# Performance work log

Measured on AMD Instinct MI355X. Metric: run time of the kernel, lower is better.

## Reference

```python
import jax, jax.numpy as jnp
from jax import lax
import numpy as np

O = 64      # out_channels (== in_channels == groups, depthwise)
P = 3       # prompt_len
K = 17      # prompt_size (large kernel size)
RANK = 4
# (small_kernel_size, pixel_unshuffle_scale, dilations) for prompt_size=17
CONFIGS = [(3, 4, (4, 5, 7)), (5, 2, (1,)), (9, 1, (2,))]


def conv2d(x, w, b=None, stride=1, padding=0, dilation=1, groups=1):
    out = lax.conv_general_dilated(
        x, w, (stride, stride), [(padding, padding)] * 2,
        rhs_dilation=(dilation, dilation), feature_group_count=groups,
        dimension_numbers=('NCHW', 'OIHW', 'NCHW'))
    return out if b is None else out + b[None, :, None, None]


def pixel_unshuffle(x, s):
    n, c, h, w = x.shape
    x = x.reshape(n, c, h // s, s, w // s, s)
    return x.transpose(0, 1, 3, 5, 2, 4).reshape(n, c * s * s, h // s, w // s)


def bilinear(x, oh, ow):
    # F.interpolate(mode='bilinear', align_corners=False); all uses downsample
    n, c, h, w = x.shape
    def coords(o, i):
        src = jnp.clip((jnp.arange(o, dtype=jnp.float32) + 0.5) * (i / o) - 0.5, 0.0, i - 1.0)
        i0 = jnp.floor(src).astype(jnp.int32)
        i1 = jnp.minimum(i0 + 1, i - 1)
        return i0, i1, src - i0.astype(jnp.float32)
    y0, y1, ty = coords(oh, h)
    x0, x1, tx = coords(ow, w)
    r0, r1 = x[:, :, y0], x[:, :, y1]
    top = r0[:, :, :, x0] * (1 - tx) + r0[:, :, :, x1] * tx
    bot = r1[:, :, :, x0] * (1 - tx) + r1[:, :, :, x1] * tx
    ty = ty[:, None]
    return top * (1 - ty) + bot * ty


def zero_interleave(k, d):
    # conv_transpose2d with 1x1 ones kernel, stride d == insert d-1 zeros
    o, c, ks, _ = k.shape
    e = d * (ks - 1) + 1
    return jnp.zeros((o, c, e, e), k.dtype).at[:, :, ::d, ::d].set(k)


def _branch(weight0, k_size, scale, dils, dw_w, dw_b, w1, b1, w2, b2, dilw, merged):
    w = weight0
    if scale > 1:
        ph = (-K) % scale
        w = jnp.pad(w, ((0, 0), (0, 0), (0, ph), (0, ph)))
        w = pixel_unshuffle(w, scale)
    h = conv2d(w, dw_w, dw_b, padding=1, groups=dw_w.shape[0])  # depthwise 3x3
    h = jax.nn.relu(conv2d(h, w1, b1))                          # 1x1 expand
    h = conv2d(h, w2, b2)                                       # 1x1 project
    h = bilinear(h, k_size, k_size)                             # (O, P*scale_or_P, k, k)
    for idx, d in enumerate(dils):
        dk = jnp.einsum('ochw,pc->ophw', h, dilw[idx])          # 1x1, no bias -> (O,P,k,k)
        eq = zero_interleave(dk, d)
        p = K // 2 - eq.shape[-1] // 2
        merged = merged + jnp.pad(eq, ((0, 0), (0, 0), (p, p), (p, p)))
    return merged


def _forward(x, A1, A2, A3, B1, B2, B3,
             dw_w3, dw_b3, w1_3, b1_3, w2_3, b2_3, dilw3,
             dw_w5, dw_b5, w1_5, b1_5, w2_5, b2_5, dilw5,
             dw_w9, dw_b9, w1_9, b1_9, w2_9, b2_9, dilw9):
    # low-rank reconstruction: (O,1,K,r) @ (O,1,r,K) -> (O,1,K,K), cat -> (O,P,K,K)
    weight0 = jnp.concatenate(
        [jnp.einsum('oikj,oijl->oikl', A, B) for A, B in ((A1, B1), (A2, B2), (A3, B3))],
        axis=1)
    merged = jnp.zeros_like(weight0)
    packs = [(dw_w3, dw_b3, w1_3, b1_3, w2_3, b2_3, dilw3),
             (dw_w5, dw_b5, w1_5, b1_5, w2_5, b2_5, dilw5),
             (dw_w9, dw_b9, w1_9, b1_9, w2_9, b2_9, dilw9)]
    for (k_size, scale, dils), pk in zip(CONFIGS, packs):
        merged = _branch(weight0, k_size, scale, dils, *pk, merged)
    w = merged.reshape(O * P, 1, K, K)
    return conv2d(x, w, padding=K // 2, groups=64)  # depthwise, 3 filters per channel


def setup_inputs() -> dict:
    key = jax.random.key(0)
    ks = iter(jax.random.split(key, 64))
    def rn(shape, s=0.05):
        return jax.random.normal(next(ks), shape, jnp.float32) * s
    inp = {'x': jax.random.normal(next(ks), (8, 64, 256, 256), jnp.float32)}
    for i in (1, 2, 3):
        inp[f'A{i}'] = rn((O, 1, K, RANK), 0.2)
        inp[f'B{i}'] = rn((O, 1, RANK, K), 0.2)
    # (pixel_unshuffle channels, hidden, mlp_out, n_dilations) per kernel size
    specs = {3: (48, 64, 12, 3), 5: (12, 48, 6, 1), 9: (3, 12, 3, 1)}
    for kk, (c, hid, out_c, nd) in specs.items():
        inp[f'dw_w{kk}'] = rn((c, 1, 3, 3))
        inp[f'dw_b{kk}'] = rn((c,))
        inp[f'w1_{kk}'] = rn((hid, c, 1, 1))
        inp[f'b1_{kk}'] = rn((hid,))
        inp[f'w2_{kk}'] = rn((out_c, hid, 1, 1))
        inp[f'b2_{kk}'] = rn((out_c,))
        inp[f'dilw{kk}'] = rn((nd, P, out_c))
    return inp


def reference(x, A1, A2, A3, B1, B2, B3,
              dw_w3, dw_b3, w1_3, b1_3, w2_3, b2_3, dilw3,
              dw_w5, dw_b5, w1_5, b1_5, w2_5, b2_5, dilw5,
              dw_w9, dw_b9, w1_9, b1_9, w2_9, b2_9, dilw9):
    return _forward(x, A1, A2, A3, B1, B2, B3,
                    dw_w3, dw_b3, w1_3, b1_3, w2_3, b2_3, dilw3,
                    dw_w5, dw_b5, w1_5, b1_5, w2_5, b2_5, dilw5,
                    dw_w9, dw_b9, w1_9, b1_9, w2_9, b2_9, dilw9)
```

## Files before the change

kernel.cpp:

```cpp
#include <hip/hip_runtime.h>
#include <cstddef>

typedef _Float16 h8 __attribute__((ext_vector_type(8)));
typedef float f4 __attribute__((ext_vector_type(4)));
typedef unsigned int uint32;

struct BranchP {
  int ksz, scale, CIN, HID, COUT, S, nd;
  int dils[3];
  const float *dw_w, *dw_b, *w1, *b1, *w2, *b2, *dilw;
};

__device__ void run_branch(int tid, const BranchP P,
                           const float* w0, float* merged,
                           float* bufA, float* bufB) {
  const int S = P.S, ksz = P.ksz, CIN = P.CIN, HID = P.HID, COUT = P.COUT;
  const int SS = S * S;
  for (int i = tid; i < CIN * SS; i += 256) {
    const int cc = i / SS, rem = i % SS, hh = rem / S, ww = rem % S;
    const int s2 = P.scale * P.scale;
    const int c = cc / s2, r2 = cc % s2, si = r2 / P.scale, sj = r2 % P.scale;
    const int sh = hh * P.scale + si, sw = ww * P.scale + sj;
    bufA[i] = (sh < 17 && sw < 17) ? w0[c * 289 + sh * 17 + sw] : 0.f;
  }
  __syncthreads();
  for (int i = tid; i < CIN * SS; i += 256) {
    const int ch = i / SS, rem = i % SS, y = rem / S, x = rem % S;
    float acc = P.dw_b[ch];
    for (int u = 0; u < 3; ++u)
      for (int v = 0; v < 3; ++v) {
        const int yy = y + u - 1, xx = x + v - 1;
        if (yy >= 0 && yy < S && xx >= 0 && xx < S)
          acc += bufA[ch * SS + yy * S + xx] * P.dw_w[ch * 9 + u * 3 + v];
      }
    bufB[i] = acc;
  }
  __syncthreads();
  for (int i = tid; i < HID * SS; i += 256) {
    const int ho = i / SS, rem = i % SS;
    float acc = P.b1[ho];
    for (int ci = 0; ci < CIN; ++ci) acc += bufB[ci * SS + rem] * P.w1[ho * CIN + ci];
    bufA[i] = fmaxf(acc, 0.f);
  }
  __syncthreads();
  for (int i = tid; i < COUT * SS; i += 256) {
    const int po = i / SS, rem = i % SS;
    float acc = P.b2[po];
    for (int ci = 0; ci < HID; ++ci) acc += bufA[ci * SS + rem] * P.w2[po * HID + ci];
    bufB[i] = acc;
  }
  __syncthreads();
  for (int i = tid; i < COUT * ksz * ksz; i += 256) {
    const int c = i / (ksz * ksz), rem = i % (ksz * ksz), oy = rem / ksz, ox = rem % ksz;
    const float ratio = (float)S / (float)ksz;
    float sy = fminf(fmaxf((oy + 0.5f) * ratio - 0.5f, 0.f), (float)(S - 1));
    float sx = fminf(fmaxf((ox + 0.5f) * ratio - 0.5f, 0.f), (float)(S - 1));
    const int y0 = (int)sy; const int y1 = min(y0 + 1, S - 1); const float ty = sy - (float)y0;
    const int x0 = (int)sx; const int x1 = min(x0 + 1, S - 1); const float tx = sx - (float)x0;
    const float* img = bufB + c * SS;
    const float top = img[y0 * S + x0] * (1.f - tx) + img[y0 * S + x1] * tx;
    const float bot = img[y1 * S + x0] * (1.f - tx) + img[y1 * S + x1] * tx;
    bufA[i] = top * (1.f - ty) + bot * ty;
  }
  __syncthreads();
  for (int di = 0; di < P.nd; ++di) {
    const int d = P.dils[di];
    const int e = d * (ksz - 1) + 1, pp = 8 - e / 2;
    for (int i = tid; i < 3 * ksz * ksz; i += 256) {
      const int p = i / (ksz * ksz), rem = i % (ksz * ksz), ih = rem / ksz, iw = rem % ksz;
      float acc = 0.f;
      for (int c2 = 0; c2 < COUT; ++c2)
        acc += bufA[c2 * ksz * ksz + rem] * P.dilw[(di * 3 + p) * COUT + c2];
      merged[p * 289 + (pp + d * ih) * 17 + (pp + d * iw)] += acc;
    }
  }
  __syncthreads();
}

#define KPAD 416
#define ACH (2 * 16 * KPAD)

__global__ __launch_bounds__(256) void prep_kernel(
    const float* __restrict__ A1, const float* __restrict__ B1,
    const float* __restrict__ A2, const float* __restrict__ B2,
    const float* __restrict__ A3, const float* __restrict__ B3,
    const float* __restrict__ dw_w3, const float* __restrict__ dw_b3,
    const float* __restrict__ w1_3, const float* __restrict__ b1_3,
    const float* __restrict__ w2_3, const float* __restrict__ b2_3,
    const float* __restrict__ dilw3,
    const float* __restrict__ dw_w5, const float* __restrict__ dw_b5,
    const float* __restrict__ w1_5, const float* __restrict__ b1_5,
    const float* __restrict__ w2_5, const float* __restrict__ b2_5,
    const float* __restrict__ dilw5,
    const float* __restrict__ dw_w9, const float* __restrict__ dw_b9,
    const float* __restrict__ w1_9, const float* __restrict__ b1_9,
    const float* __restrict__ w2_9, const float* __restrict__ b2_9,
    const float* __restrict__ dilw9,
    _Float16* __restrict__ wA) {
  const int o = blockIdx.x;
  const int tid = threadIdx.x;
  __shared__ float w0[3 * 289];
  __shared__ float merged[3 * 289];
  __shared__ float bufA[3888];
  __shared__ float bufB[3888];

  for (int i = tid; i < 3 * 289; i += 256) {
    const int c = i / 289, rem = i % 289, k = rem / 17, l = rem % 17;
    const float* A = (c == 0 ? A1 : (c == 1 ? A2 : A3)) + o * 68;
    const float* B = (c == 0 ? B1 : (c == 1 ? B2 : B3)) + o * 68;
    float s = 0.f;
    for (int r = 0; r < 4; ++r) s += A[k * 4 + r] * B[r * 17 + l];
    w0[i] = s;
    merged[i] = 0.f;
  }
  __syncthreads();

  {
    BranchP P{3, 4, 48, 64, 12, 5, 3, {4, 5, 7}, dw_w3, dw_b3, w1_3, b1_3, w2_3, b2_3, dilw3};
    run_branch(tid, P, w0, merged, bufA, bufB);
  }
  {
    BranchP P{5, 2, 12, 48, 6, 9, 1, {1, 0, 0}, dw_w5, dw_b5, w1_5, b1_5, w2_5, b2_5, dilw5};
    run_branch(tid, P, w0, merged, bufA, bufB);
  }
  {
    BranchP P{9, 1, 3, 12, 3, 17, 1, {2, 0, 0}, dw_w9, dw_b9, w1_9, b1_9, w2_9, b2_9, dilw9};
    run_branch(tid, P, w0, merged, bufA, bufB);
  }

  for (int i = tid; i < ACH; i += 256) {
    const int g = i / (16 * KPAD);
    const int m = (i / KPAD) % 16;
    const int k = i % KPAD;
    const int dxi = k / 24, r = k % 24;
    int pp, yo;
    if (g == 0) { pp = m & 1; yo = m >> 1; } else { pp = 2; yo = m; }
    const int dy = r - 8 - yo;
    float val = 0.f;
    if (!(g == 1 && m >= 8) && dy >= -8 && dy <= 8 && dxi <= 16)
      val = merged[pp * 289 + (dy + 8) * 17 + dxi];
    wA[(size_t)o * ACH + i] = (_Float16)val;
  }
}

__global__ __launch_bounds__(256) void conv_mfma_kernel(
    const float* __restrict__ xin, const _Float16* __restrict__ wA,
    float* __restrict__ out) {
  const int wid = ((blockIdx.x & 7) << 9) + (blockIdx.x >> 3);
  const int n   = wid >> 9;
  const int ch  = (wid >> 3) & 63;
  const int yg  = (wid & 7) * 32;
  const int tid = threadIdx.x;

#define PITCH 56
  __shared__ __align__(16) _Float16 Xt[280 * PITCH];

  const float* xim = xin + ((size_t)(n * 64 + ch)) * 65536;

  const int lane = tid & 63;
  const int wv = tid >> 6;
  const int row = lane & 15;
  const int kg = lane >> 4;

  h8 a1[13], a2[13];
  {
    const _Float16* Ab = wA + (size_t)ch * ACH + row * KPAD;
    #pragma unroll
    for (int t = 0; t < 13; ++t) {
      const int k0 = t * 32 + kg * 8;
      a1[t] = __builtin_bit_cast(h8, *(const uint4*)(Ab + k0));
      a2[t] = __builtin_bit_cast(h8, *(const uint4*)(Ab + 16 * KPAD + k0));
    }
  }

  for (int i = tid; i < 4 * 280; i += 256) {
    const int rb = i / 280, c = i % 280;
    const int gx = c - 8;
    const bool cok = (gx >= 0 && gx < 256);
    float v[8];
    #pragma unroll
    for (int rr = 0; rr < 8; ++rr) {
      const int gy = yg - 8 + rb * 8 + rr;
      v[rr] = (cok && gy >= 0 && gy < 256) ? xim[gy * 256 + gx] : 0.f;
    }
    uint4 u;
    u.x = __builtin_bit_cast(uint32, __builtin_amdgcn_cvt_pkrtz(v[0], v[1]));
    u.y = __builtin_bit_cast(uint32, __builtin_amdgcn_cvt_pkrtz(v[2], v[3]));
    u.z = __builtin_bit_cast(uint32, __builtin_amdgcn_cvt_pkrtz(v[4], v[5]));
    u.w = __builtin_bit_cast(uint32, __builtin_amdgcn_cvt_pkrtz(v[6], v[7]));
    *(uint4*)&Xt[c * PITCH + rb * 8] = u;
  }
  __syncthreads();

  float pbv[3][8];
  int pbc[3], pbrb[3];
  #pragma unroll
  for (int q = 0; q < 3; ++q) {
    const int i = tid + q * 256;
    pbc[q] = -1;
    if (i < 2 * 280) {
      const int rb = 4 + i / 280, c = i % 280;
      pbc[q] = c; pbrb[q] = rb;
      const int gx = c - 8;
      const bool cok = (gx >= 0 && gx < 256);
      #pragma unroll
      for (int rr = 0; rr < 8; ++rr) {
        const int gy = yg - 8 + rb * 8 + rr;
        pbv[q][rr] = (cok && gy >= 0 && gy < 256) ? xim[gy * 256 + gx] : 0.f;
      }
    }
  }

  int boff[13];
  #pragma unroll
  for (int t = 0; t < 13; ++t) {
    const int k0 = t * 32 + kg * 8;
    const int dxi = k0 / 24, r0 = k0 - dxi * 24;
    boff[t] = (row + dxi) * PITCH + r0;
  }

#define DO_PAIR(pr) do {                                                       \
    const int g_ = (pr) >> 1, cp_ = (pr) & 1;                                  \
    const int j0a_ = (wv * 4 + cp_ * 2) * 16;                                  \
    const int ba_ = j0a_ * PITCH + 8 * g_;                                     \
    const int bb_ = ba_ + 16 * PITCH;                                          \
    f4 c1a = {0.f,0.f,0.f,0.f}, c2a = {0.f,0.f,0.f,0.f};                       \
    f4 c1b = {0.f,0.f,0.f,0.f}, c2b = {0.f,0.f,0.f,0.f};                       \
    _Pragma("unroll")                                                          \
    for (int t = 0; t < 13; ++t) {                                             \
      const h8 vba = __builtin_bit_cast(h8, *(const uint4*)&Xt[ba_ + boff[t]]);\
      const h8 vbb = __builtin_bit_cast(h8, *(const uint4*)&Xt[bb_ + boff[t]]);\
      c1a = __builtin_amdgcn_mfma_f32_16x16x32_f16(a1[t], vba, c1a, 0, 0, 0);  \
      c1b = __builtin_amdgcn_mfma_f32_16x16x32_f16(a1[t], vbb, c1b, 0, 0, 0);  \
      c2a = __builtin_amdgcn_mfma_f32_16x16x32_f16(a2[t], vba, c2a, 0, 0, 0);  \
      c2b = __builtin_amdgcn_mfma_f32_16x16x32_f16(a2[t], vbb, c2b, 0, 0, 0);  \
    }                                                                          \
    const int ygg_ = yg + 8 * g_;                                              \
    _Pragma("unroll")                                                          \
    for (int half = 0; half < 2; ++half) {                                     \
      const int gx_ = j0a_ + half * 16 + row;                                  \
      const f4 s1 = half ? c1b : c1a;                                          \
      const f4 s2 = half ? c2b : c2a;                                          \
      _Pragma("unroll")                                                        \
      for (int reg = 0; reg < 4; ++reg) {                                      \
        const int r_ = kg * 4 + reg;                                           \
        out[(((size_t)n * 192 + ch * 3 + (r_ & 1)) * 256 + (ygg_ + (r_ >> 1))) * 256 + gx_] = s1[reg]; \
      }                                                                        \
      if (kg < 2) {                                                            \
        _Pragma("unroll")                                                      \
        for (int reg = 0; reg < 4; ++reg) {                                    \
          const int r_ = kg * 4 + reg;                                         \
          out[(((size_t)n * 192 + ch * 3 + 2) * 256 + (ygg_ + r_)) * 256 + gx_] = s2[reg]; \
        }                                                                      \
      }                                                                        \
    }                                                                          \
  } while (0)

  DO_PAIR(0); DO_PAIR(1);

  #pragma unroll
  for (int q = 0; q < 3; ++q) {
    if (pbc[q] >= 0) {
      uint4 u;
      u.x = __builtin_bit_cast(uint32, __builtin_amdgcn_cvt_pkrtz(pbv[q][0], pbv[q][1]));
      u.y = __builtin_bit_cast(uint32, __builtin_amdgcn_cvt_pkrtz(pbv[q][2], pbv[q][3]));
      u.z = __builtin_bit_cast(uint32, __builtin_amdgcn_cvt_pkrtz(pbv[q][4], pbv[q][5]));
      u.w = __builtin_bit_cast(uint32, __builtin_amdgcn_cvt_pkrtz(pbv[q][6], pbv[q][7]));
      *(uint4*)&Xt[pbc[q] * PITCH + pbrb[q] * 8] = u;
    }
  }

  DO_PAIR(2); DO_PAIR(3);

  __syncthreads();

  DO_PAIR(4); DO_PAIR(5); DO_PAIR(6); DO_PAIR(7);

#undef DO_PAIR
#undef PITCH
}

extern "C" void kernel_launch(void* const* d_in, const int* in_sizes, int n_in,
                              void* d_out, int out_size, void* d_ws, size_t ws_size,
                              hipStream_t stream) {
  const float* xin = (const float*)d_in[0];
  const float* A1 = (const float*)d_in[1];
  const float* B1 = (const float*)d_in[2];
  const float* A2 = (const float*)d_in[3];
  const float* B2 = (const float*)d_in[4];
  const float* A3 = (const float*)d_in[5];
  const float* B3 = (const float*)d_in[6];
  const float* dw_w3 = (const float*)d_in[7];
  const float* dw_b3 = (const float*)d_in[8];
  const float* w1_3 = (const float*)d_in[9];
  const float* b1_3 = (const float*)d_in[10];
  const float* w2_3 = (const float*)d_in[11];
  const float* b2_3 = (const float*)d_in[12];
  const float* dilw3 = (const float*)d_in[13];
  const float* dw_w5 = (const float*)d_in[14];
  const float* dw_b5 = (const float*)d_in[15];
  const float* w1_5 = (const float*)d_in[16];
  const float* b1_5 = (const float*)d_in[17];
  const float* w2_5 = (const float*)d_in[18];
  const float* b2_5 = (const float*)d_in[19];
  const float* dilw5 = (const float*)d_in[20];
  const float* dw_w9 = (const float*)d_in[21];
  const float* dw_b9 = (const float*)d_in[22];
  const float* w1_9 = (const float*)d_in[23];
  const float* b1_9 = (const float*)d_in[24];
  const float* w2_9 = (const float*)d_in[25];
  const float* b2_9 = (const float*)d_in[26];
  const float* dilw9 = (const float*)d_in[27];

  _Float16* wA = (_Float16*)d_ws;

  prep_kernel<<<64, 256, 0, stream>>>(
      A1, B1, A2, B2, A3, B3,
      dw_w3, dw_b3, w1_3, b1_3, w2_3, b2_3, dilw3,
      dw_w5, dw_b5, w1_5, b1_5, w2_5, b2_5, dilw5,
      dw_w9, dw_b9, w1_9, b1_9, w2_9, b2_9, dilw9,
      wA);

  conv_mfma_kernel<<<dim3(4096), 256, 0, stream>>>(xin, wA, (float*)d_out);
}
```

Before: 214.4 us.

## Cut register pressure: stream second weight tile from memory, drop split prefetch

The second A-operand weight tile is no longer kept in registers. It is reloaded from global memory in staged groups inside each pair computation, and the kernel now asks for 3 blocks per SM via launch bounds. The register prefetch of the lower input rows, with its mid-kernel LDS write and extra barrier, is replaced by loading all 6 row blocks before a single barrier. The aim is to free VGPRs for higher occupancy. The cost is repeated global/L2 weight loads per pair and the loss of overlap between the second input load and the MFMA work.

```diff
diff --git a/kernel.cpp b/kernel.cpp
--- a/kernel.cpp
+++ b/kernel.cpp
@@ -143,7 +143,7 @@
   }
 }
 
-__global__ __launch_bounds__(256) void conv_mfma_kernel(
+__global__ __launch_bounds__(256, 3) void conv_mfma_kernel(
     const float* __restrict__ xin, const _Float16* __restrict__ wA,
     float* __restrict__ out) {
   const int wid = ((blockIdx.x & 7) << 9) + (blockIdx.x >> 3);
@@ -162,18 +162,14 @@
   const int row = lane & 15;
   const int kg = lane >> 4;
 
-  h8 a1[13], a2[13];
-  {
-    const _Float16* Ab = wA + (size_t)ch * ACH + row * KPAD;
-    #pragma unroll
-    for (int t = 0; t < 13; ++t) {
-      const int k0 = t * 32 + kg * 8;
-      a1[t] = __builtin_bit_cast(h8, *(const uint4*)(Ab + k0));
-      a2[t] = __builtin_bit_cast(h8, *(const uint4*)(Ab + 16 * KPAD + k0));
-    }
-  }
-
-  for (int i = tid; i < 4 * 280; i += 256) {
+  const _Float16* Ab = wA + (size_t)ch * ACH + row * KPAD;
+  const _Float16* A2p = Ab + 16 * KPAD + kg * 8;
+  h8 a1[13];
+  #pragma unroll
+  for (int t = 0; t < 13; ++t)
+    a1[t] = __builtin_bit_cast(h8, *(const uint4*)(Ab + t * 32 + kg * 8));
+
+  for (int i = tid; i < 6 * 280; i += 256) {
     const int rb = i / 280, c = i % 280;
     const int gx = c - 8;
     const bool cok = (gx >= 0 && gx < 256);
@@ -192,25 +188,6 @@
   }
   __syncthreads();
 
-  float pbv[3][8];
-  int pbc[3], pbrb[3];
-  #pragma unroll
-  for (int q = 0; q < 3; ++q) {
-    const int i = tid + q * 256;
-    pbc[q] = -1;
-    if (i < 2 * 280) {
-      const int rb = 4 + i / 280, c = i % 280;
-      pbc[q] = c; pbrb[q] = rb;
-      const int gx = c - 8;
-      const bool cok = (gx >= 0 && gx < 256);
-      #pragma unroll
-      for (int rr = 0; rr < 8; ++rr) {
-        const int gy = yg - 8 + rb * 8 + rr;
-        pbv[q][rr] = (cok && gy >= 0 && gy < 256) ? xim[gy * 256 + gx] : 0.f;
-      }
-    }
-  }
-
   int boff[13];
   #pragma unroll
   for (int t = 0; t < 13; ++t) {
@@ -218,6 +195,17 @@
     const int dxi = k0 / 24, r0 = k0 - dxi * 24;
     boff[t] = (row + dxi) * PITCH + r0;
   }
+
+#define A2LD(t) __builtin_bit_cast(h8, *(const uint4*)(A2p + (t) * 32))
+
+#define MSTEP(t, a2v) do {                                                     \
+    const h8 vba = __builtin_bit_cast(h8, *(const uint4*)&Xt[ba_ + boff[t]]);  \
+    const h8 vbb = __builtin_bit_cast(h8, *(const uint4*)&Xt[bb_ + boff[t]]);  \
+    c1a = __builtin_amdgcn_mfma_f32_16x16x32_f16(a1[t], vba, c1a, 0, 0, 0);    \
+    c1b = __builtin_amdgcn_mfma_f32_16x16x32_f16(a1[t], vbb, c1b, 0, 0, 0);    \
+    c2a = __builtin_amdgcn_mfma_f32_16x16x32_f16((a2v), vba, c2a, 0, 0, 0);    \
+    c2b = __builtin_amdgcn_mfma_f32_16x16x32_f16((a2v), vbb, c2b, 0, 0, 0);    \
+  } while (0)
 
 #define DO_PAIR(pr) do {                                                       \
     const int g_ = (pr) >> 1, cp_ = (pr) & 1;                                  \
@@ -226,57 +214,41 @@
     const int bb_ = ba_ + 16 * PITCH;                                          \
     f4 c1a = {0.f,0.f,0.f,0.f}, c2a = {0.f,0.f,0.f,0.f};                       \
     f4 c1b = {0.f,0.f,0.f,0.f}, c2b = {0.f,0.f,0.f,0.f};                       \
-    _Pragma("unroll")                                                          \
-    for (int t = 0; t < 13; ++t) {                                             \
-      const h8 vba = __builtin_bit_cast(h8, *(const uint4*)&Xt[ba_ + boff[t]]);\
-      const h8 vbb = __builtin_bit_cast(h8, *(const uint4*)&Xt[bb_ + boff[t]]);\
-      c1a = __builtin_amdgcn_mfma_f32_16x16x32_f16(a1[t], vba, c1a, 0, 0, 0);  \
-      c1b = __builtin_amdgcn_mfma_f32_16x16x32_f16(a1[t], vbb, c1b, 0, 0, 0);  \
-      c2a = __builtin_amdgcn_mfma_f32_16x16x32_f16(a2[t], vba, c2a, 0, 0, 0);  \
-      c2b = __builtin_amdgcn_mfma_f32_16x16x32_f16(a2[t], vbb, c2b, 0, 0, 0);  \
-    }                                                                          \
+    h8 s0 = A2LD(0), s1 = A2LD(1), s2 = A2LD(2), s3 = A2LD(3);                 \
+    h8 s4 = A2LD(4), s5 = A2LD(5), s6 = A2LD(6);                               \
+    MSTEP(0, s0); MSTEP(1, s1); MSTEP(2, s2); MSTEP(3, s3);                    \
+    s0 = A2LD(7); s1 = A2LD(8); s2 = A2LD(9);                                  \
+    s3 = A2LD(10); h8 s7 = A2LD(11), s8 = A2LD(12);                            \
+    MSTEP(4, s4); MSTEP(5, s5); MSTEP(6, s6);                                  \
+    MSTEP(7, s0); MSTEP(8, s1); MSTEP(9, s2);                                  \
+    MSTEP(10, s3); MSTEP(11, s7); MSTEP(12, s8);                               \
     const int ygg_ = yg + 8 * g_;                                              \
     _Pragma("unroll")                                                          \
     for (int half = 0; half < 2; ++half) {                                     \
       const int gx_ = j0a_ + half * 16 + row;                                  \
-      const f4 s1 = half ? c1b : c1a;                                          \
-      const f4 s2 = half ? c2b : c2a;                                          \
+      const f4 t1 = half ? c1b : c1a;                                          \
+      const f4 t2 = half ? c2b : c2a;                                          \
       _Pragma("unroll")                                                        \
       for (int reg = 0; reg < 4; ++reg) {                                      \
         const int r_ = kg * 4 + reg;                                           \
-        out[(((size_t)n * 192 + ch * 3 + (r_ & 1)) * 256 + (ygg_ + (r_ >> 1))) * 256 + gx_] = s1[reg]; \
+        out[(((size_t)n * 192 + ch * 3 + (r_ & 1)) * 256 + (ygg_ + (r_ >> 1))) * 256 + gx_] = t1[reg]; \
       }                                                                        \
       if (kg < 2) {                                                            \
         _Pragma("unroll")                                                      \
         for (int reg = 0; reg < 4; ++reg) {                                    \
           const int r_ = kg * 4 + reg;                                         \
-          out[(((size_t)n * 192 + ch * 3 + 2) * 256 + (ygg_ + r_)) * 256 + gx_] = s2[reg]; \
+          out[(((size_t)n * 192 + ch * 3 + 2) * 256 + (ygg_ + r_)) * 256 + gx_] = t2[reg]; \
         }                                                                      \
       }                                                                        \
     }                                                                          \
   } while (0)
 
-  DO_PAIR(0); DO_PAIR(1);
-
-  #pragma unroll
-  for (int q = 0; q < 3; ++q) {
-    if (pbc[q] >= 0) {
-      uint4 u;
-      u.x = __builtin_bit_cast(uint32, __builtin_amdgcn_cvt_pkrtz(pbv[q][0], pbv[q][1]));
-      u.y = __builtin_bit_cast(uint32, __builtin_amdgcn_cvt_pkrtz(pbv[q][2], pbv[q][3]));
-      u.z = __builtin_bit_cast(uint32, __builtin_amdgcn_cvt_pkrtz(pbv[q][4], pbv[q][5]));
-      u.w = __builtin_bit_cast(uint32, __builtin_amdgcn_cvt_pkrtz(pbv[q][6], pbv[q][7]));
-      *(uint4*)&Xt[pbc[q] * PITCH + pbrb[q] * 8] = u;
-    }
-  }
-
-  DO_PAIR(2); DO_PAIR(3);
-
-  __syncthreads();
-
+  DO_PAIR(0); DO_PAIR(1); DO_PAIR(2); DO_PAIR(3);
   DO_PAIR(4); DO_PAIR(5); DO_PAIR(6); DO_PAIR(7);
 
 #undef DO_PAIR
+#undef MSTEP
+#undef A2LD
 #undef PITCH
 }
 
```

New measurement: 240.1 us. 1.12x slower.
